# Performance work log

Hardware: AMD Instinct MI355X
Metric: run time of the kernel (lower is better)

Reference implementation:

```python
import jax, jax.numpy as jnp
import numpy as np

N = 1024      # codeword length (input_size == output_size)
H1 = 3072     # edges of Tanner graph 1
H2 = 4096     # edges of Tanner graph 2
D1 = 6        # per-row mask degree, graph 1
D2 = 8        # per-row mask degree, graph 2
B = 2048      # batch
CLIP = 0.999999


def _row_indices(rng, rows, cols, deg):
    # deg distinct column indices per row (nonzeros of the binary CN mask)
    u = rng.random((rows, cols))
    return np.argsort(u, axis=1)[:, :deg].astype(np.int32)


def setup_inputs() -> dict:
    key = jax.random.key(0)
    ks = jax.random.split(key, 12)
    rng = np.random.default_rng(0)
    x = jax.random.normal(ks[0], (B, N), dtype=jnp.float32) * 2.0
    # CN-update masks as index lists
    idx1_first = jnp.asarray(_row_indices(rng, H1, N, D1))
    idx1_mid = jnp.asarray(_row_indices(rng, H1, H1, D1))
    idx2_first = jnp.asarray(_row_indices(rng, H2, N, D2))
    idx2_mid = jnp.asarray(_row_indices(rng, H2, H2, D2))
    # VN-update weights: xavier-like init pre-multiplied by sparse binary mask
    def sparse_w(k, shape, p):
        k1, k2 = jax.random.split(k)
        w = jax.random.normal(k1, shape, dtype=jnp.float32) * (1.0 / np.sqrt(shape[1]))
        m = (jax.random.uniform(k2, shape) < p).astype(jnp.float32)
        return w * m
    Wv1 = jnp.stack([sparse_w(jax.random.fold_in(ks[1], i), (H1, H1), 0.01) for i in range(5)])
    Wout1 = jnp.stack([sparse_w(jax.random.fold_in(ks[2], i), (N, H1), 0.01) for i in range(5)])
    Wv2 = jnp.stack([sparse_w(jax.random.fold_in(ks[3], i), (H2, H2), 0.01) for i in range(5)])
    Wout2 = jnp.stack([sparse_w(jax.random.fold_in(ks[4], i), (N, H2), 0.01) for i in range(5)])
    # bias scaling vectors: init eye(N) in the torch module; small perturbation to avoid triviality
    S = jnp.stack([jnp.eye(N, dtype=jnp.float32)
                   + 0.01 * jax.random.normal(jax.random.fold_in(ks[5], i), (N, N), dtype=jnp.float32)
                   for i in range(10)])
    B1 = jax.random.normal(ks[6], (N, H1), dtype=jnp.float32) * 0.02
    B2 = jax.random.normal(ks[7], (N, H2), dtype=jnp.float32) * 0.02
    return {"x": x, "S": S, "B1": B1, "B2": B2,
            "Wv1": Wv1, "Wout1": Wout1, "Wv2": Wv2, "Wout2": Wout2,
            "idx1_first": idx1_first, "idx1_mid": idx1_mid,
            "idx2_first": idx2_first, "idx2_mid": idx2_mid}


def cn_update(x, idx):
    # x: (B, in), idx: (out, deg) -> (B, out)
    vals = x[:, idx]                                   # (B, out, deg) gather
    nz = vals != 0.0
    prod = jnp.prod(jnp.where(nz, vals, 1.0), axis=-1)  # zeros act as 1
    return jnp.where(jnp.any(nz, axis=-1), prod, 0.0)   # all-zero rows -> 0


def reference(x, S, B1, B2, Wv1, Wout1, Wv2, Wout2,
              idx1_first, idx1_mid, idx2_first, idx2_mid):
    llrs = []
    for k in range(10):  # 10 unrolled BP iterations, alternating the two graphs
        g1 = (k % 2 == 0)
        j = k // 2
        Bm = B1 if g1 else B2
        Wv = Wv1[j] if g1 else Wv2[j]
        Wo = Wout1[j] if g1 else Wout2[j]
        idf = idx1_first if g1 else idx2_first
        idm = idx1_mid if g1 else idx2_mid
        chS = x @ S[k]                                  # Channel_LLR @ bias_scaling
        t = jnp.tanh(0.5 * x)
        t = jnp.clip(cn_update(t, idf), -CLIP, CLIP)
        t = 2.0 * jnp.arctanh(t)
        t = jnp.tanh(0.5 * (t @ Wv.T + chS @ Bm))
        t = jnp.clip(cn_update(t, idm), -CLIP, CLIP)
        t = 2.0 * jnp.arctanh(t)
        x = t @ Wo.T + chS
        llrs.append(jax.nn.sigmoid(x))
    return tuple(llrs)
```

## Files before the change

kernel.cpp:

```cpp
#include <hip/hip_runtime.h>
#include <hip/hip_bf16.h>
#include <stdint.h>
#include <stddef.h>

using bf16 = __hip_bfloat16;
typedef __attribute__((ext_vector_type(8))) short short8;
typedef __attribute__((ext_vector_type(2))) float f32x2;
typedef __attribute__((ext_vector_type(4))) float f32x4;
typedef __attribute__((ext_vector_type(4))) unsigned u32x4;

constexpr int BATCH = 2048;
constexpr int NN    = 1024;
constexpr int H1C   = 3072;
constexpr int H2C   = 4096;
constexpr int CAP   = 128;
constexpr int CHS_GB = (NN / 128) * (BATCH / 64);
constexpr int NPAN  = 8;
constexpr int PW    = BATCH / NPAN;

constexpr int ROW_WV1 = 0;
constexpr int ROW_WO1 = 5 * H1C;
constexpr int ROW_WV2 = ROW_WO1 + 5 * NN;
constexpr int ROW_WO2 = ROW_WV2 + 5 * H2C;
constexpr int ROWS_TOTAL = ROW_WO2 + 5 * NN;

__device__ __forceinline__ unsigned short f2bf(float f) {
  unsigned u = __float_as_uint(f);
  unsigned r = 0x7FFFu + ((u >> 16) & 1u);
  return (unsigned short)((u + r) >> 16);
}
__device__ __forceinline__ float bf2f(short s) {
  return __uint_as_float(((unsigned)(unsigned short)s) << 16);
}

__device__ __forceinline__ unsigned phi_enc_f8(float x) {
  const float e = expf(-fabsf(x));
  const float phi = logf((1.f + e) / (1.f - e));
  const unsigned sgn = __float_as_uint(x) >> 31;
  const float v = __uint_as_float(__float_as_uint(phi) | (sgn << 31));
  const int pk = __builtin_amdgcn_cvt_pk_fp8_f32(v, v, 0, false);
  const unsigned b = (unsigned)pk & 0xFFu;
  return (x == 0.f) ? 0x7Fu : b;
}

__device__ __forceinline__ void gload16(const void* g, void* lds_base) {
  __builtin_amdgcn_global_load_lds(
      (const __attribute__((address_space(1))) void*)g,
      (__attribute__((address_space(3))) void*)lds_base, 16, 0, 0);
}

template<int D>
__device__ __forceinline__ void cn_math_f8(const int2* v, float* rs) {
  float s[8];
  unsigned sg[8];
  bool any[8];
#pragma unroll
  for (int e = 0; e < 8; ++e) { s[e] = 0.f; sg[e] = 0u; any[e] = false; }
#pragma unroll
  for (int d = 0; d < D; ++d) {
    const f32x2 q0 = __builtin_amdgcn_cvt_pk_f32_fp8(v[d].x, false);
    const f32x2 q1 = __builtin_amdgcn_cvt_pk_f32_fp8(v[d].x, true);
    const f32x2 q2 = __builtin_amdgcn_cvt_pk_f32_fp8(v[d].y, false);
    const f32x2 q3 = __builtin_amdgcn_cvt_pk_f32_fp8(v[d].y, true);
    const float mag[8] = { fabsf(q0[0]), fabsf(q0[1]), fabsf(q1[0]), fabsf(q1[1]),
                           fabsf(q2[0]), fabsf(q2[1]), fabsf(q3[0]), fabsf(q3[1]) };
    const unsigned wx = (unsigned)v[d].x, wy = (unsigned)v[d].y;
#pragma unroll
    for (int e = 0; e < 8; ++e) {
      const unsigned byte = ((e < 4 ? wx : wy) >> (8 * (e & 3))) & 0xFFu;
      const bool nz = ((byte & 0x7Fu) != 0x7Fu);
      any[e] |= nz;
      s[e] += nz ? mag[e] : 0.f;
      sg[e] ^= byte >> 7;
    }
  }
#pragma unroll
  for (int e = 0; e < 8; ++e) {
    const float y = fmaxf(s[e], 1.0000005e-6f);
    const float u = expf(-y);
    float r = logf((1.f + u) / (1.f - u));
    r = any[e] ? r : 0.f;
    rs[e] = __uint_as_float(__float_as_uint(r) | (sg[e] << 31));
  }
}

__device__ __forceinline__ void cn_store_fp8(const float* rs, uint8_t* dst) {
  int lo = 0, hi = 0;
  lo = __builtin_amdgcn_cvt_pk_fp8_f32(rs[0], rs[1], lo, false);
  lo = __builtin_amdgcn_cvt_pk_fp8_f32(rs[2], rs[3], lo, true);
  hi = __builtin_amdgcn_cvt_pk_fp8_f32(rs[4], rs[5], hi, false);
  hi = __builtin_amdgcn_cvt_pk_fp8_f32(rs[6], rs[7], hi, true);
  int2 o; o.x = lo; o.y = hi;
  *(int2*)dst = o;
}

template<int D>
__global__ __launch_bounds__(256, 2) void chs_cn(
    const bf16* __restrict__ A, const bf16* __restrict__ BT,
    float* __restrict__ C, bf16* __restrict__ Cb, const float* __restrict__ add,
    const uint8_t* __restrict__ src, const int* __restrict__ idx,
    uint8_t* __restrict__ outf8)
{
  __shared__ bf16 As[64 * 32];
  __shared__ bf16 Bs[128 * 32];
  const int bid = blockIdx.x;
  const int tid = threadIdx.x;
  if (bid < CHS_GB) {
    const int lane = tid & 63;
    const int w    = tid >> 6;
    const int bn = bid & 7;
    const int bm = bid >> 3;
    const int wn = w * 32;
    const int l15 = lane & 15;
    const int lk  = (lane >> 4) * 8;
    const int ld4 = (lane >> 4) * 4;
    const int sr  = lane >> 2;
    const int kc  = (lane & 3) * 8;

    f32x4 acc[4][2];
#pragma unroll
    for (int i = 0; i < 4; ++i)
#pragma unroll
      for (int j = 0; j < 2; ++j)
#pragma unroll
        for (int e = 0; e < 4; ++e) acc[i][j][e] = 0.f;

    const size_t rA = (size_t)bm * 64;
    const size_t rB = (size_t)bn * 128;

    for (int kt = 0; kt < NN; kt += 32) {
#pragma unroll
      for (int c = 0; c < 3; ++c) {
        const int slot = w * 3 + c;
        if (slot < 4) {
          const int r = slot * 16 + sr;
          gload16(A + (rA + r) * (size_t)NN + kt + kc, &As[slot * 512]);
        } else {
          const int r = (slot - 4) * 16 + sr;
          gload16(BT + (rB + r) * (size_t)NN + kt + kc, &Bs[(slot - 4) * 512]);
        }
      }
      __syncthreads();
      short8 af[4], bfr[2];
#pragma unroll
      for (int f = 0; f < 4; ++f)
        af[f] = *(const short8*)&As[(f * 16 + l15) * 32 + lk];
#pragma unroll
      for (int f = 0; f < 2; ++f)
        bfr[f] = *(const short8*)&Bs[(wn + f * 16 + l15) * 32 + lk];
#pragma unroll
      for (int i = 0; i < 4; ++i)
#pragma unroll
        for (int j = 0; j < 2; ++j)
          acc[i][j] = __builtin_amdgcn_mfma_f32_16x16x32_bf16(af[i], bfr[j], acc[i][j], 0, 0, 0);
      __syncthreads();
    }

#pragma unroll
    for (int i = 0; i < 4; ++i) {
      const int row0 = bm * 64 + i * 16 + ld4;
#pragma unroll
      for (int j = 0; j < 2; ++j) {
        const int col = bn * 128 + wn + j * 16 + l15;
#pragma unroll
        for (int e = 0; e < 4; ++e) {
          const size_t o = (size_t)(row0 + e) * NN + col;
          float v = acc[i][j][e] + add[o];
          C[o] = v;
          Cb[o] = __float2bfloat16(v);
        }
      }
    }
  } else {
    const int h = bid - CHS_GB;
    const int b = tid * 8;
    const int* ir = idx + (size_t)h * D;
    int rows[D];
#pragma unroll
    for (int d = 0; d < D; ++d) rows[d] = ir[d];
    int2 v[D];
#pragma unroll
    for (int d = 0; d < D; ++d)
      v[d] = *(const int2*)(src + (size_t)rows[d] * BATCH + b);
    float rs[8];
    cn_math_f8<D>(v, rs);
    cn_store_fp8(rs, outf8 + (size_t)h * BATCH + b);
  }
}

__global__ __launch_bounds__(256, 2) void zgemm_wv(
    const bf16* __restrict__ A, const bf16* __restrict__ BT, bf16* __restrict__ Cb,
    int K, int gb,
    const uint8_t* __restrict__ t1f8,
    const unsigned* __restrict__ pack, const int* __restrict__ nnz,
    int rowoff, float* __restrict__ gTf)
{
  __shared__ bf16 As[128 * 32];
  __shared__ bf16 Bs[128 * 32];
  const int bid = blockIdx.x;
  if (bid < gb) {
    const int tid  = threadIdx.x;
    const int lane = tid & 63;
    const int w    = tid >> 6;
    const int bn = bid & 15;
    const int bm = bid >> 4;
    const int wm = (w >> 1) * 64, wn = (w & 1) * 64;
    const int l15 = lane & 15;
    const int lk  = (lane >> 4) * 8;
    const int ld4 = (lane >> 4) * 4;
    const int sr  = lane >> 2;
    const int kc  = (lane & 3) * 8;

    f32x4 acc[4][4];
#pragma unroll
    for (int i = 0; i < 4; ++i)
#pragma unroll
      for (int j = 0; j < 4; ++j)
#pragma unroll
        for (int e = 0; e < 4; ++e) acc[i][j][e] = 0.f;

    const size_t rA = (size_t)bm * 128;
    const size_t rB = (size_t)bn * 128;

    for (int kt = 0; kt < K; kt += 32) {
#pragma unroll
      for (int c = 0; c < 2; ++c) {
        const int slot = w * 2 + c;
        const int r = slot * 16 + sr;
        gload16(A  + (rA + r) * (size_t)K + kt + kc, &As[slot * 512]);
        gload16(BT + (rB + r) * (size_t)K + kt + kc, &Bs[slot * 512]);
      }
      __syncthreads();
      short8 af[4], bfr[4];
#pragma unroll
      for (int f = 0; f < 4; ++f) {
        af[f]  = *(const short8*)&As[(wm + f * 16 + l15) * 32 + lk];
        bfr[f] = *(const short8*)&Bs[(wn + f * 16 + l15) * 32 + lk];
      }
#pragma unroll
      for (int i = 0; i < 4; ++i)
#pragma unroll
        for (int j = 0; j < 4; ++j)
          acc[i][j] = __builtin_amdgcn_mfma_f32_16x16x32_bf16(af[i], bfr[j], acc[i][j], 0, 0, 0);
      __syncthreads();
    }

#pragma unroll
    for (int i = 0; i < 4; ++i) {
      const int row0 = bm * 128 + wm + i * 16 + ld4;
#pragma unroll
      for (int j = 0; j < 4; ++j) {
        const int col = bn * 128 + wn + j * 16 + l15;
#pragma unroll
        for (int e = 0; e < 4; ++e)
          Cb[(size_t)(row0 + e) * BATCH + col] = __float2bfloat16(acc[i][j][e]);
      }
    }
  } else {
    const int h = bid - gb;
    const int b = threadIdx.x * 8;
    const int rg = rowoff + h;
    const unsigned* pr = pack + (size_t)rg * CAP;
    const int n = nnz[rg];
    f32x4 a0 = {0.f, 0.f, 0.f, 0.f};
    f32x4 a1 = {0.f, 0.f, 0.f, 0.f};
    int j = 0;
    for (; j + 4 <= n; j += 4) {
      const u32x4 w4 = *(const u32x4*)(pr + j);
      int2 t[4];
#pragma unroll
      for (int q = 0; q < 4; ++q)
        t[q] = *(const int2*)(t1f8 + (size_t)(w4[q] & 0xFFFFu) * BATCH + b);
#pragma unroll
      for (int q = 0; q < 4; ++q) {
        const float v = bf2f((short)(w4[q] >> 16));
        const f32x2 p01 = __builtin_amdgcn_cvt_pk_f32_fp8(t[q].x, false);
        const f32x2 p23 = __builtin_amdgcn_cvt_pk_f32_fp8(t[q].x, true);
        const f32x2 p45 = __builtin_amdgcn_cvt_pk_f32_fp8(t[q].y, false);
        const f32x2 p67 = __builtin_amdgcn_cvt_pk_f32_fp8(t[q].y, true);
        a0[0] += v * p01[0]; a0[1] += v * p01[1];
        a0[2] += v * p23[0]; a0[3] += v * p23[1];
        a1[0] += v * p45[0]; a1[1] += v * p45[1];
        a1[2] += v * p67[0]; a1[3] += v * p67[1];
      }
    }
    for (; j < n; ++j) {
      const unsigned pk = pr[j];
      const float v = bf2f((short)(pk >> 16));
      const int2 t = *(const int2*)(t1f8 + (size_t)(pk & 0xFFFFu) * BATCH + b);
      const f32x2 p01 = __builtin_amdgcn_cvt_pk_f32_fp8(t.x, false);
      const f32x2 p23 = __builtin_amdgcn_cvt_pk_f32_fp8(t.x, true);
      const f32x2 p45 = __builtin_amdgcn_cvt_pk_f32_fp8(t.y, false);
      const f32x2 p67 = __builtin_amdgcn_cvt_pk_f32_fp8(t.y, true);
      a0[0] += v * p01[0]; a0[1] += v * p01[1];
      a0[2] += v * p23[0]; a0[3] += v * p23[1];
      a1[0] += v * p45[0]; a1[1] += v * p45[1];
      a1[2] += v * p67[0]; a1[3] += v * p67[1];
    }
    float* orow = gTf + (size_t)h * BATCH + b;
    *(f32x4*)orow = a0;
    *(f32x4*)(orow + 4) = a1;
  }
}

__global__ __launch_bounds__(256) void phi_add_pin(
    const unsigned short* __restrict__ zb, const float* __restrict__ gbuf,
    uint8_t* __restrict__ t2p)
{
  const int panel = blockIdx.x;
  const int w = threadIdx.x >> 6, lane = threadIdx.x & 63;
  const int h = blockIdx.y * 4 + w;
  const int b = panel * PW + lane * 4;
  const size_t o = (size_t)h * BATCH + b;
  const int2 z = *(const int2*)(zb + o);
  const f32x4 g = *(const f32x4*)(gbuf + o);
  const unsigned zx = (unsigned)z.x, zy = (unsigned)z.y;
  unsigned ov = 0;
  ov |= phi_enc_f8(bf2f((short)(zx & 0xFFFFu)) + g[0]);
  ov |= phi_enc_f8(bf2f((short)(zx >> 16))    + g[1]) << 8;
  ov |= phi_enc_f8(bf2f((short)(zy & 0xFFFFu)) + g[2]) << 16;
  ov |= phi_enc_f8(bf2f((short)(zy >> 16))    + g[3]) << 24;
  *(unsigned*)(t2p + o) = ov;
}

template<int D>
__global__ __launch_bounds__(256) void cn_pin(
    const uint8_t* __restrict__ src,
    const int* __restrict__ idx,
    uint8_t* __restrict__ out)
{
  const int panel = blockIdx.x;
  const int w = threadIdx.x >> 6, lane = threadIdx.x & 63;
  const int h = blockIdx.y * 4 + w;
  const int b = panel * PW + lane * 4;
  const int* ir = idx + (size_t)h * D;
  int rows[D];
#pragma unroll
  for (int d = 0; d < D; ++d) rows[d] = ir[d];
  unsigned v[D];
#pragma unroll
  for (int d = 0; d < D; ++d)
    v[d] = *(const unsigned*)(src + (size_t)rows[d] * BATCH + b);
  float s[4];
  unsigned sg[4];
  bool any[4];
#pragma unroll
  for (int e = 0; e < 4; ++e) { s[e] = 0.f; sg[e] = 0u; any[e] = false; }
#pragma unroll
  for (int d = 0; d < D; ++d) {
    const f32x2 q0 = __builtin_amdgcn_cvt_pk_f32_fp8((int)v[d], false);
    const f32x2 q1 = __builtin_amdgcn_cvt_pk_f32_fp8((int)v[d], true);
    const float mag[4] = { fabsf(q0[0]), fabsf(q0[1]), fabsf(q1[0]), fabsf(q1[1]) };
#pragma unroll
    for (int e = 0; e < 4; ++e) {
      const unsigned byte = (v[d] >> (8 * e)) & 0xFFu;
      const bool nz = ((byte & 0x7Fu) != 0x7Fu);
      any[e] |= nz;
      s[e] += nz ? mag[e] : 0.f;
      sg[e] ^= byte >> 7;
    }
  }
  float rs[4];
#pragma unroll
  for (int e = 0; e < 4; ++e) {
    const float y = fmaxf(s[e], 1.0000005e-6f);
    const float u = expf(-y);
    float r = logf((1.f + u) / (1.f - u));
    r = any[e] ? r : 0.f;
    rs[e] = __uint_as_float(__float_as_uint(r) | (sg[e] << 31));
  }
  int o = 0;
  o = __builtin_amdgcn_cvt_pk_fp8_f32(rs[0], rs[1], o, false);
  o = __builtin_amdgcn_cvt_pk_fp8_f32(rs[2], rs[3], o, true);
  *(int*)(out + (size_t)h * BATCH + b) = o;
}

__global__ __launch_bounds__(256) void wo_pin(
    const uint8_t* __restrict__ t3f8,
    const unsigned* __restrict__ pack, const int* __restrict__ nnz,
    int rowoff, float* __restrict__ xp)
{
  const int panel = blockIdx.x;
  const int w = threadIdx.x >> 6, lane = threadIdx.x & 63;
  const int nrow = blockIdx.y * 4 + w;
  const int b = panel * PW + lane * 4;
  const int rg = rowoff + nrow;
  const unsigned* pr = pack + (size_t)rg * CAP;
  const int cnt = nnz[rg];
  f32x4 a = {0.f, 0.f, 0.f, 0.f};
  int j = 0;
  for (; j + 4 <= cnt; j += 4) {
    const u32x4 w4 = *(const u32x4*)(pr + j);
    unsigned t[4];
#pragma unroll
    for (int q = 0; q < 4; ++q)
      t[q] = *(const unsigned*)(t3f8 + (size_t)(w4[q] & 0xFFFFu) * BATCH + b);
#pragma unroll
    for (int q = 0; q < 4; ++q) {
      const float v = bf2f((short)(w4[q] >> 16));
      const f32x2 p01 = __builtin_amdgcn_cvt_pk_f32_fp8((int)t[q], false);
      const f32x2 p23 = __builtin_amdgcn_cvt_pk_f32_fp8((int)t[q], true);
      a[0] += v * p01[0]; a[1] += v * p01[1];
      a[2] += v * p23[0]; a[3] += v * p23[1];
    }
  }
  for (; j < cnt; ++j) {
    const unsigned pk = pr[j];
    const float v = bf2f((short)(pk >> 16));
    const unsigned t = *(const unsigned*)(t3f8 + (size_t)(pk & 0xFFFFu) * BATCH + b);
    const f32x2 p01 = __builtin_amdgcn_cvt_pk_f32_fp8((int)t, false);
    const f32x2 p23 = __builtin_amdgcn_cvt_pk_f32_fp8((int)t, true);
    a[0] += v * p01[0]; a[1] += v * p01[1];
    a[2] += v * p23[0]; a[3] += v * p23[1];
  }
  *(f32x4*)(xp + (size_t)nrow * BATCH + b) = a;
}

__global__ __launch_bounds__(256) void prep_smit(const float* __restrict__ S, bf16* __restrict__ out)
{
  __shared__ float ls[64][65];
  const int k = blockIdx.z;
  const int n0 = blockIdx.x * 64, m0 = blockIdx.y * 64;
  const float* Sk = S + (size_t)k * NN * NN;
  bf16* ok = out + (size_t)k * NN * NN;
  const int tc = threadIdx.x & 63, tr = threadIdx.x >> 6;
#pragma unroll
  for (int i = 0; i < 16; ++i) {
    const int r = tr + i * 4;
    ls[r][tc] = Sk[(size_t)(m0 + r) * NN + n0 + tc];
  }
  __syncthreads();
#pragma unroll
  for (int i = 0; i < 16; ++i) {
    const int r = tr + i * 4;
    float v = ls[tc][r] - ((m0 + tc) == (n0 + r) ? 1.f : 0.f);
    ok[(size_t)(n0 + r) * NN + m0 + tc] = __float2bfloat16(v);
  }
}

__global__ __launch_bounds__(256) void prep_bt(const float* __restrict__ Bsrc, bf16* __restrict__ out, int H)
{
  __shared__ float ls[64][65];
  const int h0 = blockIdx.x * 64, n0 = blockIdx.y * 64;
  const int tc = threadIdx.x & 63, tr = threadIdx.x >> 6;
#pragma unroll
  for (int i = 0; i < 16; ++i) {
    const int r = tr + i * 4;
    ls[r][tc] = Bsrc[(size_t)(n0 + r) * H + h0 + tc];
  }
  __syncthreads();
#pragma unroll
  for (int i = 0; i < 16; ++i) {
    const int r = tr + i * 4;
    out[(size_t)(h0 + r) * NN + n0 + tc] = __float2bfloat16(ls[tc][r]);
  }
}

__global__ __launch_bounds__(256) void csr_build(
    const float* __restrict__ W, int rowlen,
    unsigned* __restrict__ pack, int* __restrict__ nnz, int row_off)
{
  const int row = blockIdx.x;
  const float* wr = W + (size_t)row * rowlen;
  const size_t base = (size_t)(row_off + row) * CAP;
  __shared__ int wtot[4];
  __shared__ int cbase;
  if (threadIdx.x == 0) cbase = 0;
  __syncthreads();
  const int lane = threadIdx.x & 63, wv = threadIdx.x >> 6;
  const unsigned long long lanemask = (1ull << lane) - 1ull;
  for (int c0 = 0; c0 < rowlen; c0 += 1024) {
    const int c = c0 + threadIdx.x * 4;
    const f32x4 v = *(const f32x4*)(wr + c);
    unsigned long long m[4];
#pragma unroll
    for (int e = 0; e < 4; ++e) m[e] = __ballot(v[e] != 0.f);
    int pre_lane = 0;
#pragma unroll
    for (int e = 0; e < 4; ++e) pre_lane += __popcll(m[e] & lanemask);
    if (lane == 0)
      wtot[wv] = __popcll(m[0]) + __popcll(m[1]) + __popcll(m[2]) + __popcll(m[3]);
    __syncthreads();
    int pre = cbase + pre_lane;
    for (int i = 0; i < wv; ++i) pre += wtot[i];
    int off = 0;
#pragma unroll
    for (int e = 0; e < 4; ++e) {
      if (v[e] != 0.f) {
        const int p = pre + off;
        if (p < CAP) pack[base + p] = ((unsigned)f2bf(v[e]) << 16) | (unsigned)(c + e);
        ++off;
      }
    }
    __syncthreads();
    if (threadIdx.x == 0) cbase += wtot[0] + wtot[1] + wtot[2] + wtot[3];
    __syncthreads();
  }
  if (threadIdx.x == 0) nnz[row_off + row] = (cbase < CAP ? cbase : CAP);
}

__global__ __launch_bounds__(256) void fuse_out(
    const float* __restrict__ xpT,
    const float* __restrict__ chS,
    float* __restrict__ dout,
    float* __restrict__ xf,
    bf16* __restrict__ xb,
    uint8_t* __restrict__ tfT)
{
  __shared__ float lc[64][65];
  __shared__ float lx[64][65];
  const int n0 = blockIdx.x * 64, b0 = blockIdx.y * 64;
  const int tc = threadIdx.x & 63, tr = threadIdx.x >> 6;
#pragma unroll
  for (int i = 0; i < 16; ++i) {
    const int r = tr + i * 4;
    lc[r][tc] = chS[(size_t)(b0 + r) * NN + n0 + tc];
    lx[r][tc] = xpT[(size_t)(n0 + r) * BATCH + b0 + tc];
  }
  __syncthreads();
#pragma unroll
  for (int i = 0; i < 16; ++i) {
    const int r = tr + i * 4;
    const float v = lc[r][tc] + lx[tc][r];
    const size_t o = (size_t)(b0 + r) * NN + n0 + tc;
    dout[o] = 1.f / (1.f + expf(-v));
    xf[o] = v;
    xb[o] = __float2bfloat16(v);
  }
#pragma unroll
  for (int i = 0; i < 16; ++i) {
    const int r = tr + i * 4;
    const float v = lc[tc][r] + lx[r][tc];
    tfT[(size_t)(n0 + r) * BATCH + b0 + tc] = (uint8_t)phi_enc_f8(v);
  }
}

__global__ __launch_bounds__(256) void init_prep(
    const float* __restrict__ x, bf16* __restrict__ xb, uint8_t* __restrict__ tfT)
{
  __shared__ float ls[64][65];
  const int n0 = blockIdx.x * 64, b0 = blockIdx.y * 64;
  const int tc = threadIdx.x & 63, tr = threadIdx.x >> 6;
#pragma unroll
  for (int i = 0; i < 16; ++i) {
    const int r = tr + i * 4;
    const size_t o = (size_t)(b0 + r) * NN + n0 + tc;
    const float v = x[o];
    ls[r][tc] = v;
    xb[o] = __float2bfloat16(v);
  }
  __syncthreads();
#pragma unroll
  for (int i = 0; i < 16; ++i) {
    const int r = tr + i * 4;
    tfT[(size_t)(n0 + r) * BATCH + b0 + tc] = (uint8_t)phi_enc_f8(ls[tc][r]);
  }
}

extern "C" void kernel_launch(void* const* d_in, const int* in_sizes, int n_in,
                              void* d_out, int out_size, void* d_ws, size_t ws_size,
                              hipStream_t stream)
{
  const float* x_in  = (const float*)d_in[0];
  const float* S     = (const float*)d_in[1];
  const float* B1    = (const float*)d_in[2];
  const float* B2    = (const float*)d_in[3];
  const float* Wv1   = (const float*)d_in[4];
  const float* Wout1 = (const float*)d_in[5];
  const float* Wv2   = (const float*)d_in[6];
  const float* Wout2 = (const float*)d_in[7];
  const int* idx1f   = (const int*)d_in[8];
  const int* idx1m   = (const int*)d_in[9];
  const int* idx2f   = (const int*)d_in[10];
  const int* idx2m   = (const int*)d_in[11];
  float* out = (float*)d_out;

  uint8_t* p = (uint8_t*)d_ws;
  auto alloc = [&](size_t bytes) -> void* {
    void* r = p;
    p += (bytes + 255) & ~(size_t)255;
    return r;
  };
  bf16*  SmIT = (bf16*)alloc((size_t)10 * NN * NN * sizeof(bf16));
  bf16*  B1T  = (bf16*)alloc((size_t)H1C * NN * sizeof(bf16));
  bf16*  B2T  = (bf16*)alloc((size_t)H2C * NN * sizeof(bf16));
  unsigned* cpack = (unsigned*)alloc((size_t)ROWS_TOTAL * CAP * sizeof(unsigned));
  int*   cnnz  = (int*)alloc((size_t)ROWS_TOTAL * sizeof(int));
  float* xf   = (float*)alloc((size_t)BATCH * NN * sizeof(float));
  bf16*  xb   = (bf16*)alloc((size_t)BATCH * NN * sizeof(bf16));
  uint8_t* tfT = (uint8_t*)alloc((size_t)NN * BATCH);
  float* chS  = (float*)alloc((size_t)BATCH * NN * sizeof(float));
  bf16*  chSb = (bf16*)alloc((size_t)BATCH * NN * sizeof(bf16));
  uint8_t* t1f8 = (uint8_t*)alloc((size_t)H2C * BATCH);
  uint8_t* t3f8 = (uint8_t*)alloc((size_t)H2C * BATCH);
  unsigned short* zTb = (unsigned short*)alloc((size_t)H2C * BATCH * sizeof(unsigned short));
  float* gTf  = (float*)alloc((size_t)H2C * BATCH * sizeof(float));
  uint8_t* t2p = (uint8_t*)alloc((size_t)H2C * BATCH);
  float* xpT  = (float*)alloc((size_t)NN * BATCH * sizeof(float));
  (void)ws_size; (void)in_sizes; (void)n_in; (void)out_size;

  prep_smit<<<dim3(NN / 64, NN / 64, 10), 256, 0, stream>>>(S, SmIT);
  prep_bt<<<dim3(H1C / 64, NN / 64), 256, 0, stream>>>(B1, B1T, H1C);
  prep_bt<<<dim3(H2C / 64, NN / 64), 256, 0, stream>>>(B2, B2T, H2C);
  csr_build<<<5 * H1C, 256, 0, stream>>>(Wv1,   H1C, cpack, cnnz, ROW_WV1);
  csr_build<<<5 * NN,  256, 0, stream>>>(Wout1, H1C, cpack, cnnz, ROW_WO1);
  csr_build<<<5 * H2C, 256, 0, stream>>>(Wv2,   H2C, cpack, cnnz, ROW_WV2);
  csr_build<<<5 * NN,  256, 0, stream>>>(Wout2, H2C, cpack, cnnz, ROW_WO2);
  init_prep<<<dim3(NN / 64, BATCH / 64), 256, 0, stream>>>(x_in, xb, tfT);

  for (int k = 0; k < 10; ++k) {
    const bool g1 = (k % 2 == 0);
    const int j = k / 2;
    const int H = g1 ? H1C : H2C;
    const bf16* BmT = g1 ? B1T : B2T;
    const int* idf = g1 ? idx1f : idx2f;
    const int* idm = g1 ? idx1m : idx2m;
    const int wv_off = g1 ? (ROW_WV1 + j * H1C) : (ROW_WV2 + j * H2C);
    const int wo_off = g1 ? (ROW_WO1 + j * NN)  : (ROW_WO2 + j * NN);
    const float* xcur = (k == 0) ? x_in : xf;
    const int gb = (BATCH / 128) * (H / 128);

    if (g1) chs_cn<6><<<CHS_GB + H, 256, 0, stream>>>(
        xb, SmIT + (size_t)k * NN * NN, chS, chSb, xcur, tfT, idf, t1f8);
    else    chs_cn<8><<<CHS_GB + H, 256, 0, stream>>>(
        xb, SmIT + (size_t)k * NN * NN, chS, chSb, xcur, tfT, idf, t1f8);
    zgemm_wv<<<gb + H, 256, 0, stream>>>(
        BmT, chSb, (bf16*)zTb, NN, gb, t1f8, cpack, cnnz, wv_off, gTf);
    phi_add_pin<<<dim3(NPAN, H / 4), 256, 0, stream>>>(zTb, gTf, t2p);
    if (g1) cn_pin<6><<<dim3(NPAN, H / 4), 256, 0, stream>>>(t2p, idm, t3f8);
    else    cn_pin<8><<<dim3(NPAN, H / 4), 256, 0, stream>>>(t2p, idm, t3f8);
    wo_pin<<<dim3(NPAN, NN / 4), 256, 0, stream>>>(t3f8, cpack, cnnz, wo_off, xpT);
    fuse_out<<<dim3(NN / 64, BATCH / 64), 256, 0, stream>>>(
        xpT, chS, out + (size_t)k * BATCH * NN, xf, xb, tfT);
  }
}
```

Before: 1.479 ms.

## Fuse sparse Wout SpMM into output epilogue and store Wv partials as bf16

Merges the sparse Wout product (wo_pin) into the fuse_out epilogue. Each block computes a 64x64 tile of the SpMM into shared memory, which removes the xpT fp32 round trip and one launch per iteration. The Wv sparse partial sums gTf are now written and read as bf16 instead of fp32, halving that intermediate's traffic. Risks are lower occupancy and worse gather coalescing from 16-byte loads over 64 columns per row, plus extra rounding from the bf16 storage.

```diff
diff --git a/kernel.cpp b/kernel.cpp
--- a/kernel.cpp
+++ b/kernel.cpp
@@ -193,7 +193,7 @@
     int K, int gb,
     const uint8_t* __restrict__ t1f8,
     const unsigned* __restrict__ pack, const int* __restrict__ nnz,
-    int rowoff, float* __restrict__ gTf)
+    int rowoff, unsigned short* __restrict__ gTb)
 {
   __shared__ bf16 As[128 * 32];
   __shared__ bf16 Bs[128 * 32];
@@ -297,14 +297,18 @@
       a1[0] += v * p45[0]; a1[1] += v * p45[1];
       a1[2] += v * p67[0]; a1[3] += v * p67[1];
     }
-    float* orow = gTf + (size_t)h * BATCH + b;
-    *(f32x4*)orow = a0;
-    *(f32x4*)(orow + 4) = a1;
+    short8 ov;
+#pragma unroll
+    for (int e = 0; e < 4; ++e) {
+      ov[e]     = (short)f2bf(a0[e]);
+      ov[e + 4] = (short)f2bf(a1[e]);
+    }
+    *(short8*)(gTb + (size_t)h * BATCH + b) = ov;
   }
 }
 
 __global__ __launch_bounds__(256) void phi_add_pin(
-    const unsigned short* __restrict__ zb, const float* __restrict__ gbuf,
+    const unsigned short* __restrict__ zb, const unsigned short* __restrict__ gbuf,
     uint8_t* __restrict__ t2p)
 {
   const int panel = blockIdx.x;
@@ -313,13 +317,14 @@
   const int b = panel * PW + lane * 4;
   const size_t o = (size_t)h * BATCH + b;
   const int2 z = *(const int2*)(zb + o);
-  const f32x4 g = *(const f32x4*)(gbuf + o);
+  const int2 g = *(const int2*)(gbuf + o);
   const unsigned zx = (unsigned)z.x, zy = (unsigned)z.y;
+  const unsigned gx = (unsigned)g.x, gy = (unsigned)g.y;
   unsigned ov = 0;
-  ov |= phi_enc_f8(bf2f((short)(zx & 0xFFFFu)) + g[0]);
-  ov |= phi_enc_f8(bf2f((short)(zx >> 16))    + g[1]) << 8;
-  ov |= phi_enc_f8(bf2f((short)(zy & 0xFFFFu)) + g[2]) << 16;
-  ov |= phi_enc_f8(bf2f((short)(zy >> 16))    + g[3]) << 24;
+  ov |= phi_enc_f8(bf2f((short)(zx & 0xFFFFu)) + bf2f((short)(gx & 0xFFFFu)));
+  ov |= phi_enc_f8(bf2f((short)(zx >> 16))    + bf2f((short)(gx >> 16))) << 8;
+  ov |= phi_enc_f8(bf2f((short)(zy & 0xFFFFu)) + bf2f((short)(gy & 0xFFFFu))) << 16;
+  ov |= phi_enc_f8(bf2f((short)(zy >> 16))    + bf2f((short)(gy >> 16))) << 24;
   *(unsigned*)(t2p + o) = ov;
 }
 
@@ -375,45 +380,74 @@
   *(int*)(out + (size_t)h * BATCH + b) = o;
 }
 
-__global__ __launch_bounds__(256) void wo_pin(
+__global__ __launch_bounds__(256) void wo_fuse(
     const uint8_t* __restrict__ t3f8,
-    const unsigned* __restrict__ pack, const int* __restrict__ nnz,
-    int rowoff, float* __restrict__ xp)
-{
-  const int panel = blockIdx.x;
-  const int w = threadIdx.x >> 6, lane = threadIdx.x & 63;
-  const int nrow = blockIdx.y * 4 + w;
-  const int b = panel * PW + lane * 4;
-  const int rg = rowoff + nrow;
-  const unsigned* pr = pack + (size_t)rg * CAP;
-  const int cnt = nnz[rg];
-  f32x4 a = {0.f, 0.f, 0.f, 0.f};
-  int j = 0;
-  for (; j + 4 <= cnt; j += 4) {
-    const u32x4 w4 = *(const u32x4*)(pr + j);
-    unsigned t[4];
-#pragma unroll
-    for (int q = 0; q < 4; ++q)
-      t[q] = *(const unsigned*)(t3f8 + (size_t)(w4[q] & 0xFFFFu) * BATCH + b);
-#pragma unroll
-    for (int q = 0; q < 4; ++q) {
-      const float v = bf2f((short)(w4[q] >> 16));
-      const f32x2 p01 = __builtin_amdgcn_cvt_pk_f32_fp8((int)t[q], false);
-      const f32x2 p23 = __builtin_amdgcn_cvt_pk_f32_fp8((int)t[q], true);
-      a[0] += v * p01[0]; a[1] += v * p01[1];
-      a[2] += v * p23[0]; a[3] += v * p23[1];
-    }
-  }
-  for (; j < cnt; ++j) {
-    const unsigned pk = pr[j];
-    const float v = bf2f((short)(pk >> 16));
-    const unsigned t = *(const unsigned*)(t3f8 + (size_t)(pk & 0xFFFFu) * BATCH + b);
-    const f32x2 p01 = __builtin_amdgcn_cvt_pk_f32_fp8((int)t, false);
-    const f32x2 p23 = __builtin_amdgcn_cvt_pk_f32_fp8((int)t, true);
-    a[0] += v * p01[0]; a[1] += v * p01[1];
-    a[2] += v * p23[0]; a[3] += v * p23[1];
-  }
-  *(f32x4*)(xp + (size_t)nrow * BATCH + b) = a;
+    const unsigned* __restrict__ pack, const int* __restrict__ nnz, int rowoff,
+    const float* __restrict__ chS,
+    float* __restrict__ dout, float* __restrict__ xf, bf16* __restrict__ xb,
+    uint8_t* __restrict__ tfT)
+{
+  __shared__ float lx[64][65];
+  __shared__ float lc[64][65];
+  const int n0 = blockIdx.x * 64, b0 = blockIdx.y * 64;
+  const int tid = threadIdx.x;
+
+  {
+    const int r = tid >> 2;
+    const int sub = tid & 3;
+    const int bcol = b0 + sub * 16;
+    const int rg = rowoff + n0 + r;
+    const unsigned* pr = pack + (size_t)rg * CAP;
+    const int cnt = nnz[rg];
+    f32x4 a0 = {0.f,0.f,0.f,0.f}, a1 = {0.f,0.f,0.f,0.f};
+    f32x4 a2 = {0.f,0.f,0.f,0.f}, a3 = {0.f,0.f,0.f,0.f};
+    for (int j = 0; j < cnt; ++j) {
+      const unsigned pk = pr[j];
+      const float v = bf2f((short)(pk >> 16));
+      const u32x4 t = *(const u32x4*)(t3f8 + (size_t)(pk & 0xFFFFu) * BATCH + bcol);
+#pragma unroll
+      for (int q = 0; q < 4; ++q) {
+        const f32x2 plo = __builtin_amdgcn_cvt_pk_f32_fp8((int)t[q], false);
+        const f32x2 phi = __builtin_amdgcn_cvt_pk_f32_fp8((int)t[q], true);
+        f32x4* acc = (q == 0) ? &a0 : (q == 1) ? &a1 : (q == 2) ? &a2 : &a3;
+        (*acc)[0] += v * plo[0]; (*acc)[1] += v * plo[1];
+        (*acc)[2] += v * phi[0]; (*acc)[3] += v * phi[1];
+      }
+    }
+    const int c0 = sub * 16;
+#pragma unroll
+    for (int e = 0; e < 4; ++e) {
+      lx[r][c0 + e]      = a0[e];
+      lx[r][c0 + 4 + e]  = a1[e];
+      lx[r][c0 + 8 + e]  = a2[e];
+      lx[r][c0 + 12 + e] = a3[e];
+    }
+  }
+  {
+    const int tc = tid & 63, tr = tid >> 6;
+#pragma unroll
+    for (int i = 0; i < 16; ++i) {
+      const int r = tr + i * 4;
+      lc[r][tc] = chS[(size_t)(b0 + r) * NN + n0 + tc];
+    }
+  }
+  __syncthreads();
+  const int tc = tid & 63, tr = tid >> 6;
+#pragma unroll
+  for (int i = 0; i < 16; ++i) {
+    const int r = tr + i * 4;
+    const float v = lc[r][tc] + lx[tc][r];
+    const size_t o = (size_t)(b0 + r) * NN + n0 + tc;
+    dout[o] = 1.f / (1.f + expf(-v));
+    xf[o] = v;
+    xb[o] = __float2bfloat16(v);
+  }
+#pragma unroll
+  for (int i = 0; i < 16; ++i) {
+    const int r = tr + i * 4;
+    const float v = lc[tc][r] + lx[r][tc];
+    tfT[(size_t)(n0 + r) * BATCH + b0 + tc] = (uint8_t)phi_enc_f8(v);
+  }
 }
 
 __global__ __launch_bounds__(256) void prep_smit(const float* __restrict__ S, bf16* __restrict__ out)
@@ -497,42 +531,6 @@
     __syncthreads();
   }
   if (threadIdx.x == 0) nnz[row_off + row] = (cbase < CAP ? cbase : CAP);
-}
-
-__global__ __launch_bounds__(256) void fuse_out(
-    const float* __restrict__ xpT,
-    const float* __restrict__ chS,
-    float* __restrict__ dout,
-    float* __restrict__ xf,
-    bf16* __restrict__ xb,
-    uint8_t* __restrict__ tfT)
-{
-  __shared__ float lc[64][65];
-  __shared__ float lx[64][65];
-  const int n0 = blockIdx.x * 64, b0 = blockIdx.y * 64;
-  const int tc = threadIdx.x & 63, tr = threadIdx.x >> 6;
-#pragma unroll
-  for (int i = 0; i < 16; ++i) {
-    const int r = tr + i * 4;
-    lc[r][tc] = chS[(size_t)(b0 + r) * NN + n0 + tc];
-    lx[r][tc] = xpT[(size_t)(n0 + r) * BATCH + b0 + tc];
-  }
-  __syncthreads();
-#pragma unroll
-  for (int i = 0; i < 16; ++i) {
-    const int r = tr + i * 4;
-    const float v = lc[r][tc] + lx[tc][r];
-    const size_t o = (size_t)(b0 + r) * NN + n0 + tc;
-    dout[o] = 1.f / (1.f + expf(-v));
-    xf[o] = v;
-    xb[o] = __float2bfloat16(v);
-  }
-#pragma unroll
-  for (int i = 0; i < 16; ++i) {
-    const int r = tr + i * 4;
-    const float v = lc[tc][r] + lx[r][tc];
-    tfT[(size_t)(n0 + r) * BATCH + b0 + tc] = (uint8_t)phi_enc_f8(v);
-  }
 }
 
 __global__ __launch_bounds__(256) void init_prep(
@@ -594,9 +592,8 @@
   uint8_t* t1f8 = (uint8_t*)alloc((size_t)H2C * BATCH);
   uint8_t* t3f8 = (uint8_t*)alloc((size_t)H2C * BATCH);
   unsigned short* zTb = (unsigned short*)alloc((size_t)H2C * BATCH * sizeof(unsigned short));
-  float* gTf  = (float*)alloc((size_t)H2C * BATCH * sizeof(float));
+  unsigned short* gTb = (unsigned short*)alloc((size_t)H2C * BATCH * sizeof(unsigned short));
   uint8_t* t2p = (uint8_t*)alloc((size_t)H2C * BATCH);
-  float* xpT  = (float*)alloc((size_t)NN * BATCH * sizeof(float));
   (void)ws_size; (void)in_sizes; (void)n_in; (void)out_size;
 
   prep_smit<<<dim3(NN / 64, NN / 64, 10), 256, 0, stream>>>(S, SmIT);
@@ -625,12 +622,12 @@
     else    chs_cn<8><<<CHS_GB + H, 256, 0, stream>>>(
         xb, SmIT + (size_t)k * NN * NN, chS, chSb, xcur, tfT, idf, t1f8);
     zgemm_wv<<<gb + H, 256, 0, stream>>>(
-        BmT, chSb, (bf16*)zTb, NN, gb, t1f8, cpack, cnnz, wv_off, gTf);
-    phi_add_pin<<<dim3(NPAN, H / 4), 256, 0, stream>>>(zTb, gTf, t2p);
+        BmT, chSb, (bf16*)zTb, NN, gb, t1f8, cpack, cnnz, wv_off, gTb);
+    phi_add_pin<<<dim3(NPAN, H / 4), 256, 0, stream>>>(zTb, gTb, t2p);
     if (g1) cn_pin<6><<<dim3(NPAN, H / 4), 256, 0, stream>>>(t2p, idm, t3f8);
     else    cn_pin<8><<<dim3(NPAN, H / 4), 256, 0, stream>>>(t2p, idm, t3f8);
-    wo_pin<<<dim3(NPAN, NN / 4), 256, 0, stream>>>(t3f8, cpack, cnnz, wo_off, xpT);
-    fuse_out<<<dim3(NN / 64, BATCH / 64), 256, 0, stream>>>(
-        xpT, chS, out + (size_t)k * BATCH * NN, xf, xb, tfT);
-  }
-}
+    wo_fuse<<<dim3(NN / 64, BATCH / 64), 256, 0, stream>>>(
+        t3f8, cpack, cnnz, wo_off, chS,
+        out + (size_t)k * BATCH * NN, xf, xb, tfT);
+  }
+}
```

New measurement: 1.614 ms. 9.1% more time.
